# Kernel optimization log

Hardware: AMD Instinct MI355X
Metric: run time of the kernel (lower is better)

Reference implementation:

```python
import jax, jax.numpy as jnp
import numpy as np

GAMMA = 1.0
BIG = 1e10  # finite stand-in for +inf so exp/log stay NaN-free under autodiff


def _pairwise_sq_dist(X, Y):
    # X: (na, T, d), Y: (nb, T, d) -> D: (na, nb, T, T) squared euclidean
    sqx = jnp.sum(X * X, axis=-1)                      # (na, T)
    sqy = jnp.sum(Y * Y, axis=-1)                      # (nb, T)
    cross = jnp.einsum('atd,bsd->abts', X, Y)          # (na, nb, T, T)
    return sqx[:, None, :, None] + sqy[None, :, None, :] - 2.0 * cross


def _soft_dtw(D, gamma):
    # D: (B, T, T) -> (B,) soft-DTW values, anti-diagonal wavefront via lax.scan.
    B, T, _ = D.shape
    inv_g = 1.0 / gamma
    idx = jnp.arange(T)

    def step(carry, p):
        prev2, prev1 = carry                           # diagonals p-2, p-1: (B, T)
        j = p - idx
        valid = (j >= 0) & (j < T)
        d = D[:, idx, jnp.clip(j, 0, T - 1)]           # (B, T) costs on diag p
        # shifted neighbors: prev2[i-1] (diag), prev1[i-1] (up), prev1[i] (left)
        corner = jnp.where(p == 0, 0.0, BIG)           # R[0,0] = 0 boundary
        prev2_s = jnp.concatenate([jnp.broadcast_to(corner, (B, 1)), prev2[:, :-1]], axis=1)
        prev1_s = jnp.concatenate([jnp.full((B, 1), BIG, D.dtype), prev1[:, :-1]], axis=1)
        r0 = -prev2_s * inv_g
        r1 = -prev1_s * inv_g
        r2 = -prev1 * inv_g
        rmax = jnp.maximum(jnp.maximum(r0, r1), r2)
        rsum = jnp.exp(r0 - rmax) + jnp.exp(r1 - rmax) + jnp.exp(r2 - rmax)
        softmin = -gamma * (jnp.log(rsum) + rmax)
        new = jnp.where(valid[None, :], d + softmin, BIG)
        return (prev1, new), None

    init = (jnp.full((B, T), BIG, D.dtype), jnp.full((B, T), BIG, D.dtype))
    (_, last), _ = jax.lax.scan(step, init, jnp.arange(2 * T - 1))
    return last[:, T - 1]                              # R[T, T]


def setup_inputs() -> dict:
    key = jax.random.key(0)
    kx, ky = jax.random.split(key)
    X = jax.random.normal(kx, (128, 128, 8), dtype=jnp.float32)
    Y = jax.random.normal(ky, (16, 128, 8), dtype=jnp.float32)
    return {"X": X, "Y": Y}


def reference(X, Y):
    na, T, _ = X.shape
    nb = Y.shape[0]
    D = _pairwise_sq_dist(X, Y).reshape(na * nb, T, T)
    dist = _soft_dtw(D, GAMMA)
    return dist.reshape(na, nb)
```

## Files before the change

### kernel.cpp

```cpp
#include <hip/hip_runtime.h>

#define T 128
#define L2E 1.4426950408889634f
#define LN2F 0.6931471805599453f

typedef _Float16 h2 __attribute__((ext_vector_type(2)));

__device__ __forceinline__ float shr1(float x) {
    return __int_as_float(__builtin_amdgcn_update_dpp(
        0, __float_as_int(x), 0x138, 0xF, 0xF, true));
}

template <int CTRL>
__device__ __forceinline__ float dppmax(float x) {
    float t = __int_as_float(__builtin_amdgcn_update_dpp(
        __float_as_int(x), __float_as_int(x), CTRL, 0xF, 0xF, false));
    return fmaxf(x, t);
}

struct Row { float2 u, v; float s; };

__device__ __forceinline__ Row loadRow(const float* p) {
    Row r;
    r.u = *(const float2*)p;
    r.v = *(const float2*)(p + 2);
    r.s = p[4];
    return r;
}

__device__ __forceinline__ float dot2(h2 x, float ybits, float acc) {
    return __builtin_amdgcn_fdot2(x, __builtin_bit_cast(h2, ybits), acc, false);
}

__launch_bounds__(256)
__global__ void sdtw_kernel(const float* __restrict__ X,
                            const float* __restrict__ Y,
                            float* __restrict__ out) {
    __shared__ __align__(16) float lds[4 * 2304];
    const int lane = threadIdx.x & 63;
    const int w    = threadIdx.x >> 6;
    const int pair = blockIdx.x * 4 + w;
    const int a = pair >> 4;
    const int b = pair & 15;

    float* yw = lds + w * 2304;

    {
        const float* ybase = Y + (size_t)b * T * 8;
        for (int r = lane; r < 383; r += 64) {
            float4 pk; pk.x = 0.f; pk.y = 0.f; pk.z = 0.f; pk.w = 0.f;
            float sq = -3.0e37f;
            int j = r - 126;
            if (j >= 0 && j < T) {
                const float4* src = (const float4*)(ybase + j * 8);
                float4 y0 = src[0], y1 = src[1];
                float s = y0.x*y0.x + y0.y*y0.y + y0.z*y0.z + y0.w*y0.w
                        + y1.x*y1.x + y1.y*y1.y + y1.z*y1.z + y1.w*y1.w;
                const float c = 2.0f * L2E;
                h2 a0 = { (_Float16)(c*y0.x), (_Float16)(c*y0.y) };
                h2 a1 = { (_Float16)(c*y0.z), (_Float16)(c*y0.w) };
                h2 a2 = { (_Float16)(c*y1.x), (_Float16)(c*y1.y) };
                h2 a3 = { (_Float16)(c*y1.z), (_Float16)(c*y1.w) };
                pk.x = __builtin_bit_cast(float, a0);
                pk.y = __builtin_bit_cast(float, a1);
                pk.z = __builtin_bit_cast(float, a2);
                pk.w = __builtin_bit_cast(float, a3);
                sq = -L2E * s;
            }
            float* dst = yw + r * 6;
            float2 h; h.x = pk.x; h.y = pk.y;
            float2 g; g.x = pk.z; g.y = pk.w;
            *(float2*)dst = h;
            *(float2*)(dst + 2) = g;
            dst[4] = sq;
        }
    }

    h2 xe0, xe1, xe2, xe3, xo0, xo1, xo2, xo3;
    float lsxe, lsxo;
    {
        const float* xb = X + ((size_t)a * T + 2 * lane) * 8;
        const float4* s0 = (const float4*)xb;
        float4 v0 = s0[0], v1 = s0[1], u0 = s0[2], u1 = s0[3];
        xe0 = h2{ (_Float16)v0.x, (_Float16)v0.y };
        xe1 = h2{ (_Float16)v0.z, (_Float16)v0.w };
        xe2 = h2{ (_Float16)v1.x, (_Float16)v1.y };
        xe3 = h2{ (_Float16)v1.z, (_Float16)v1.w };
        lsxe = -L2E * (v0.x*v0.x+v0.y*v0.y+v0.z*v0.z+v0.w*v0.w
                      +v1.x*v1.x+v1.y*v1.y+v1.z*v1.z+v1.w*v1.w);
        xo0 = h2{ (_Float16)u0.x, (_Float16)u0.y };
        xo1 = h2{ (_Float16)u0.z, (_Float16)u0.w };
        xo2 = h2{ (_Float16)u1.x, (_Float16)u1.y };
        xo3 = h2{ (_Float16)u1.z, (_Float16)u1.w };
        lsxo = -L2E * (u0.x*u0.x+u0.y*u0.y+u0.z*u0.z+u0.w*u0.w
                      +u1.x*u1.x+u1.y*u1.y+u1.z*u1.z+u1.w*u1.w);
    }

    __syncthreads();

    Row ra = loadRow(yw + (126 - 2 * lane) * 6);
    Row rb = loadRow(yw + (127 - 2 * lane) * 6);
    Row rc = loadRow(yw + (128 - 2 * lane) * 6);
    Row rd;
    const float* fptr = yw + (129 - 2 * lane) * 6;

    float fe0 = 0.f, fo0 = 0.f, fo1 = 0.f;
    int off = 90;
    float fe1;
    {
        float acc = lsxe + ra.s;
        acc = dot2(xe0, ra.u.x, acc);
        acc = dot2(xe1, ra.u.y, acc);
        acc = dot2(xe2, ra.v.x, acc);
        acc = dot2(xe3, ra.v.y, acc);
        fe1 = __builtin_amdgcn_exp2f(acc) * 0x1p90f;
    }

#define BODY(PE1, PE2, PO1, PO2, RO, RE, RF) {          \
    RF = loadRow(fptr); fptr += 6;                      \
    float sB = shr1(PO1);                               \
    float sA = shr1(PO2);                               \
    float ae = lsxe + RE.s;                             \
    ae = dot2(xe0, RE.u.x, ae);                         \
    ae = dot2(xe1, RE.u.y, ae);                         \
    ae = dot2(xe2, RE.v.x, ae);                         \
    ae = dot2(xe3, RE.v.y, ae);                         \
    float ao = lsxo + RO.s;                             \
    ao = dot2(xo0, RO.u.x, ao);                         \
    ao = dot2(xo1, RO.u.y, ao);                         \
    ao = dot2(xo2, RO.v.x, ao);                         \
    ao = dot2(xo3, RO.v.y, ao);                         \
    float Ee = __builtin_amdgcn_exp2f(ae);              \
    float Eo = __builtin_amdgcn_exp2f(ao);              \
    float Se = Ee * ((sA + sB) + PE1);                  \
    float So = Eo * ((PE2 + PE1) + PO1);                \
    PE2 = Se; PO2 = So;                                 \
}

#define RENORM() {                                                            \
    float mx = fmaxf(fmaxf(fe0, fe1), fmaxf(fo0, fo1));                       \
    mx = dppmax<0x111>(mx);                                    \
    mx = dppmax<0x112>(mx);                                    \
    mx = dppmax<0x114>(mx);                                    \
    mx = dppmax<0x118>(mx);                                    \
    int r0_ = __builtin_amdgcn_readlane(__float_as_int(mx), 15);              \
    int r1_ = __builtin_amdgcn_readlane(__float_as_int(mx), 31);              \
    int r2_ = __builtin_amdgcn_readlane(__float_as_int(mx), 47);              \
    int r3_ = __builtin_amdgcn_readlane(__float_as_int(mx), 63);              \
    int mb = max(max(r0_, r1_), max(r2_, r3_));                               \
    int e = ((mb >> 23) & 0xff) - 217;                \
    fe0 = ldexpf(fe0, -e); fe1 = ldexpf(fe1, -e);                             \
    fo0 = ldexpf(fo0, -e); fo1 = ldexpf(fo1, -e);                             \
    off -= e;                                                                 \
}

    for (int g = 0; g < 63; ++g) {
        BODY(fe1, fe0, fo1, fo0, ra, rb, rd);
        BODY(fe0, fe1, fo0, fo1, rb, rc, ra);
        BODY(fe1, fe0, fo1, fo0, rc, rd, rb);
        BODY(fe0, fe1, fo0, fo1, rd, ra, rc);
        RENORM();
    }
    BODY(fe1, fe0, fo1, fo0, ra, rb, rd);
    BODY(fe0, fe1, fo0, fo1, rb, rc, ra);

    if (lane == 63)
        out[pair] = ((float)off - __builtin_amdgcn_logf(fo1)) * LN2F;
}

extern "C" void kernel_launch(void* const* d_in, const int* in_sizes, int n_in,
                              void* d_out, int out_size, void* d_ws, size_t ws_size,
                              hipStream_t stream) {
    const float* X = (const float*)d_in[0];
    const float* Y = (const float*)d_in[1];
    float* out = (float*)d_out;
    sdtw_kernel<<<512, 256, 0, stream>>>(X, Y, out);
}
```

Before: 86.50 us.

## Software-pipeline distance/exp stage ahead of recurrence with split even/odd LDS layout

Moves the Y-row LDS table into separate even/odd float4 arrays plus scalar arrays, so each row is read with one 16-byte load and one scalar load instead of three loads. The dot-product and exp2 for the next diagonal step are computed one step ahead of the serial recurrence, taking that latency off the loop-carried dependency chain. Each dot product is also split into two independent accumulator chains to shorten latency. In exchange it uses more registers for the extra prefetched row sets and the precomputed exponentials.

```diff
diff --git a/kernel.cpp b/kernel.cpp
--- a/kernel.cpp
+++ b/kernel.cpp
@@ -18,39 +18,38 @@
     return fmaxf(x, t);
 }
 
-struct Row { float2 u, v; float s; };
-
-__device__ __forceinline__ Row loadRow(const float* p) {
-    Row r;
-    r.u = *(const float2*)p;
-    r.v = *(const float2*)(p + 2);
-    r.s = p[4];
-    return r;
-}
-
 __device__ __forceinline__ float dot2(h2 x, float ybits, float acc) {
     return __builtin_amdgcn_fdot2(x, __builtin_bit_cast(h2, ybits), acc, false);
 }
+
+struct Pair { float4 ye; float se; float4 yo; float so; };
 
 __launch_bounds__(256)
 __global__ void sdtw_kernel(const float* __restrict__ X,
                             const float* __restrict__ Y,
                             float* __restrict__ out) {
-    __shared__ __align__(16) float lds[4 * 2304];
+    __shared__ float4 EYs[4][196];
+    __shared__ float  ESs[4][196];
+    __shared__ float4 OYs[4][196];
+    __shared__ float  OSs[4][196];
     const int lane = threadIdx.x & 63;
     const int w    = threadIdx.x >> 6;
     const int pair = blockIdx.x * 4 + w;
     const int a = pair >> 4;
     const int b = pair & 15;
 
-    float* yw = lds + w * 2304;
+    const float4* eyw = EYs[w];
+    const float*  esw = ESs[w];
+    const float4* oyw = OYs[w];
+    const float*  osw = OSs[w];
 
     {
         const float* ybase = Y + (size_t)b * T * 8;
-        for (int r = lane; r < 383; r += 64) {
+        for (int idx = lane; idx < 392; idx += 64) {
+            int P = idx & 1, h = idx >> 1;
+            int j = 2 * h + P - 126;
             float4 pk; pk.x = 0.f; pk.y = 0.f; pk.z = 0.f; pk.w = 0.f;
             float sq = -3.0e37f;
-            int j = r - 126;
             if (j >= 0 && j < T) {
                 const float4* src = (const float4*)(ybase + j * 8);
                 float4 y0 = src[0], y1 = src[1];
@@ -67,12 +66,8 @@
                 pk.w = __builtin_bit_cast(float, a3);
                 sq = -L2E * s;
             }
-            float* dst = yw + r * 6;
-            float2 h; h.x = pk.x; h.y = pk.y;
-            float2 g; g.x = pk.z; g.y = pk.w;
-            *(float2*)dst = h;
-            *(float2*)(dst + 2) = g;
-            dst[4] = sq;
+            if (P) { OYs[w][h] = pk; OSs[w][h] = sq; }
+            else   { EYs[w][h] = pk; ESs[w][h] = sq; }
         }
     }
 
@@ -80,8 +75,8 @@
     float lsxe, lsxo;
     {
         const float* xb = X + ((size_t)a * T + 2 * lane) * 8;
-        const float4* s0 = (const float4*)xb;
-        float4 v0 = s0[0], v1 = s0[1], u0 = s0[2], u1 = s0[3];
+        const float4* s0p = (const float4*)xb;
+        float4 v0 = s0p[0], v1 = s0p[1], u0 = s0p[2], u1 = s0p[3];
         xe0 = h2{ (_Float16)v0.x, (_Float16)v0.y };
         xe1 = h2{ (_Float16)v0.z, (_Float16)v0.w };
         xe2 = h2{ (_Float16)v1.x, (_Float16)v1.y };
@@ -98,43 +93,32 @@
 
     __syncthreads();
 
-    Row ra = loadRow(yw + (126 - 2 * lane) * 6);
-    Row rb = loadRow(yw + (127 - 2 * lane) * 6);
-    Row rc = loadRow(yw + (128 - 2 * lane) * 6);
-    Row rd;
-    const float* fptr = yw + (129 - 2 * lane) * 6;
+    const int hb0 = 63 - lane;
 
-    float fe0 = 0.f, fo0 = 0.f, fo1 = 0.f;
-    int off = 90;
-    float fe1;
-    {
-        float acc = lsxe + ra.s;
-        acc = dot2(xe0, ra.u.x, acc);
-        acc = dot2(xe1, ra.u.y, acc);
-        acc = dot2(xe2, ra.v.x, acc);
-        acc = dot2(xe3, ra.v.y, acc);
-        fe1 = __builtin_amdgcn_exp2f(acc) * 0x1p90f;
-    }
+#define LD_OE(SET, HE, HO) { SET.ye = oyw[HE]; SET.se = osw[HE]; \
+                             SET.yo = eyw[HO]; SET.so = esw[HO]; }
+#define LD_EO(SET, HE, HO) { SET.ye = eyw[HE]; SET.se = esw[HE]; \
+                             SET.yo = oyw[HO]; SET.so = osw[HO]; }
 
-#define BODY(PE1, PE2, PO1, PO2, RO, RE, RF) {          \
-    RF = loadRow(fptr); fptr += 6;                      \
-    float sB = shr1(PO1);                               \
-    float sA = shr1(PO2);                               \
-    float ae = lsxe + RE.s;                             \
-    ae = dot2(xe0, RE.u.x, ae);                         \
-    ae = dot2(xe1, RE.u.y, ae);                         \
-    ae = dot2(xe2, RE.v.x, ae);                         \
-    ae = dot2(xe3, RE.v.y, ae);                         \
-    float ao = lsxo + RO.s;                             \
-    ao = dot2(xo0, RO.u.x, ao);                         \
-    ao = dot2(xo1, RO.u.y, ao);                         \
-    ao = dot2(xo2, RO.v.x, ao);                         \
-    ao = dot2(xo3, RO.v.y, ao);                         \
-    float Ee = __builtin_amdgcn_exp2f(ae);              \
-    float Eo = __builtin_amdgcn_exp2f(ao);              \
-    float Se = Ee * ((sA + sB) + PE1);                  \
-    float So = Eo * ((PE2 + PE1) + PO1);                \
-    PE2 = Se; PO2 = So;                                 \
+#define DSTAGE(EE, EO, SET) {                                \
+    float t0 = dot2(xe0, SET.ye.x, lsxe);                    \
+    float t1 = dot2(xe1, SET.ye.y, SET.se);                  \
+    t0 = dot2(xe2, SET.ye.z, t0);                            \
+    t1 = dot2(xe3, SET.ye.w, t1);                            \
+    EE = __builtin_amdgcn_exp2f(t0 + t1);                    \
+    float u0 = dot2(xo0, SET.yo.x, lsxo);                    \
+    float u1 = dot2(xo1, SET.yo.y, SET.so);                  \
+    u0 = dot2(xo2, SET.yo.z, u0);                            \
+    u1 = dot2(xo3, SET.yo.w, u1);                            \
+    EO = __builtin_amdgcn_exp2f(u0 + u1);                    \
+}
+
+#define RSTAGE(PE1, PE2, PO1, PO2, EE, EO) {                 \
+    float sB = shr1(PO1);                                    \
+    float sA = shr1(PO2);                                    \
+    float Se = EE * ((sA + sB) + PE1);                       \
+    float So = EO * ((PE2 + PE1) + PO1);                     \
+    PE2 = Se; PO2 = So;                                      \
 }
 
 #define RENORM() {                                                            \
@@ -154,15 +138,47 @@
     off -= e;                                                                 \
 }
 
+    Pair S1, S2, S3, S4;
+    LD_OE(S1, hb0,     hb0);
+    LD_EO(S2, hb0 + 1, hb0);
+    LD_OE(S3, hb0 + 1, hb0 + 1);
+    LD_EO(S4, hb0 + 2, hb0 + 1);
+
+    float fe0 = 0.f, fo0 = 0.f, fo1 = 0.f, fe1;
+    int off = 90;
+    {
+        float4 yv = eyw[hb0];
+        float  sv = esw[hb0];
+        float t0 = dot2(xe0, yv.x, lsxe);
+        float t1 = dot2(xe1, yv.y, sv);
+        t0 = dot2(xe2, yv.z, t0);
+        t1 = dot2(xe3, yv.w, t1);
+        fe1 = __builtin_amdgcn_exp2f(t0 + t1) * 0x1p90f;
+    }
+    float EeA, EoA, EeB, EoB;
+    DSTAGE(EeA, EoA, S1);
+
+    int hb = hb0;
     for (int g = 0; g < 63; ++g) {
-        BODY(fe1, fe0, fo1, fo0, ra, rb, rd);
-        BODY(fe0, fe1, fo0, fo1, rb, rc, ra);
-        BODY(fe1, fe0, fo1, fo0, rc, rd, rb);
-        BODY(fe0, fe1, fo0, fo1, rd, ra, rc);
+        RSTAGE(fe1, fe0, fo1, fo0, EeA, EoA);
+        DSTAGE(EeB, EoB, S2);
+        LD_OE(S1, hb + 2, hb + 2);
+        RSTAGE(fe0, fe1, fo0, fo1, EeB, EoB);
+        DSTAGE(EeA, EoA, S3);
+        LD_EO(S2, hb + 3, hb + 2);
+        RSTAGE(fe1, fe0, fo1, fo0, EeA, EoA);
+        DSTAGE(EeB, EoB, S4);
+        LD_OE(S3, hb + 3, hb + 3);
+        RSTAGE(fe0, fe1, fo0, fo1, EeB, EoB);
+        DSTAGE(EeA, EoA, S1);
+        LD_EO(S4, hb + 4, hb + 3);
         RENORM();
+        hb += 2;
     }
-    BODY(fe1, fe0, fo1, fo0, ra, rb, rd);
-    BODY(fe0, fe1, fo0, fo1, rb, rc, ra);
+
+    RSTAGE(fe1, fe0, fo1, fo0, EeA, EoA);
+    DSTAGE(EeB, EoB, S2);
+    RSTAGE(fe0, fe1, fo0, fo1, EeB, EoB);
 
     if (lane == 63)
         out[pair] = ((float)off - __builtin_amdgcn_logf(fo1)) * LN2F;
```

Measured after the change: 88.91 us. +2.8%, slower.

## Stream Y rows through lanes via DPP shift instead of per-lane LDS loads

Applied to the files above, without the earlier changes.

Replaces the per-lane, per-step LDS row loads at lane-dependent offsets with a shift register. The Y rows ripple across lanes through DPP row-shift merges, and only lane 0 takes a fresh row, which all lanes read as a broadcast from the same LDS address. LDS rows are padded to 8 floats and batched as 8 wave-uniform loads per group, separated from the compute by a sched_barrier. The dot products are split into two independent accumulators to shorten the dependency chain. In exchange, each step adds five DPP moves and more register pressure from the eight preloaded rows.

```diff
diff --git a/kernel.cpp b/kernel.cpp
--- a/kernel.cpp
+++ b/kernel.cpp
@@ -3,12 +3,18 @@
 #define T 128
 #define L2E 1.4426950408889634f
 #define LN2F 0.6931471805599453f
+#define SENT -3.0e37f
 
 typedef _Float16 h2 __attribute__((ext_vector_type(2)));
 
 __device__ __forceinline__ float shr1(float x) {
     return __int_as_float(__builtin_amdgcn_update_dpp(
         0, __float_as_int(x), 0x138, 0xF, 0xF, true));
+}
+
+__device__ __forceinline__ float mrg(float fresh, float chain) {
+    return __int_as_float(__builtin_amdgcn_update_dpp(
+        __float_as_int(fresh), __float_as_int(chain), 0x138, 0xF, 0xF, false));
 }
 
 template <int CTRL>
@@ -18,41 +24,33 @@
     return fmaxf(x, t);
 }
 
-struct Row { float2 u, v; float s; };
-
-__device__ __forceinline__ Row loadRow(const float* p) {
-    Row r;
-    r.u = *(const float2*)p;
-    r.v = *(const float2*)(p + 2);
-    r.s = p[4];
-    return r;
-}
-
 __device__ __forceinline__ float dot2(h2 x, float ybits, float acc) {
     return __builtin_amdgcn_fdot2(x, __builtin_bit_cast(h2, ybits), acc, false);
 }
+
+struct Row { float4 y; float s; };
 
 __launch_bounds__(256)
 __global__ void sdtw_kernel(const float* __restrict__ X,
                             const float* __restrict__ Y,
                             float* __restrict__ out) {
-    __shared__ __align__(16) float lds[4 * 2304];
+    __shared__ __align__(16) float lds[4][2048];
     const int lane = threadIdx.x & 63;
     const int w    = threadIdx.x >> 6;
     const int pair = blockIdx.x * 4 + w;
     const int a = pair >> 4;
     const int b = pair & 15;
 
-    float* yw = lds + w * 2304;
+    float* yw = lds[w];
 
     {
         const float* ybase = Y + (size_t)b * T * 8;
-        for (int r = lane; r < 383; r += 64) {
+        for (int k = 0; k < 4; ++k) {
+            int r = lane + 64 * k;
             float4 pk; pk.x = 0.f; pk.y = 0.f; pk.z = 0.f; pk.w = 0.f;
-            float sq = -3.0e37f;
-            int j = r - 126;
-            if (j >= 0 && j < T) {
-                const float4* src = (const float4*)(ybase + j * 8);
+            float sq = SENT;
+            if (r < T) {
+                const float4* src = (const float4*)(ybase + r * 8);
                 float4 y0 = src[0], y1 = src[1];
                 float s = y0.x*y0.x + y0.y*y0.y + y0.z*y0.z + y0.w*y0.w
                         + y1.x*y1.x + y1.y*y1.y + y1.z*y1.z + y1.w*y1.w;
@@ -67,12 +65,10 @@
                 pk.w = __builtin_bit_cast(float, a3);
                 sq = -L2E * s;
             }
-            float* dst = yw + r * 6;
-            float2 h; h.x = pk.x; h.y = pk.y;
-            float2 g; g.x = pk.z; g.y = pk.w;
-            *(float2*)dst = h;
-            *(float2*)(dst + 2) = g;
-            dst[4] = sq;
+            float* dst = yw + r * 8;
+            *(float4*)dst = pk;
+            float4 t; t.x = sq; t.y = 0.f; t.z = 0.f; t.w = 0.f;
+            *(float4*)(dst + 4) = t;
         }
     }
 
@@ -80,8 +76,8 @@
     float lsxe, lsxo;
     {
         const float* xb = X + ((size_t)a * T + 2 * lane) * 8;
-        const float4* s0 = (const float4*)xb;
-        float4 v0 = s0[0], v1 = s0[1], u0 = s0[2], u1 = s0[3];
+        const float4* s0p = (const float4*)xb;
+        float4 v0 = s0p[0], v1 = s0p[1], u0 = s0p[2], u1 = s0p[3];
         xe0 = h2{ (_Float16)v0.x, (_Float16)v0.y };
         xe1 = h2{ (_Float16)v0.z, (_Float16)v0.w };
         xe2 = h2{ (_Float16)v1.x, (_Float16)v1.y };
@@ -98,43 +94,58 @@
 
     __syncthreads();
 
-    Row ra = loadRow(yw + (126 - 2 * lane) * 6);
-    Row rb = loadRow(yw + (127 - 2 * lane) * 6);
-    Row rc = loadRow(yw + (128 - 2 * lane) * 6);
-    Row rd;
-    const float* fptr = yw + (129 - 2 * lane) * 6;
-
-    float fe0 = 0.f, fo0 = 0.f, fo1 = 0.f;
+    Row A, B;
+    {
+        float4 r0y = *(const float4*)(yw);
+        float  r0s = yw[4];
+        bool l0 = (lane == 0);
+        A.y.x = l0 ? r0y.x : 0.f;
+        A.y.y = l0 ? r0y.y : 0.f;
+        A.y.z = l0 ? r0y.z : 0.f;
+        A.y.w = l0 ? r0y.w : 0.f;
+        A.s   = l0 ? r0s   : SENT;
+        B.y.x = 0.f; B.y.y = 0.f; B.y.z = 0.f; B.y.w = 0.f;
+        B.s   = SENT;
+    }
+
+    float fe0 = 0.f, fo0 = 0.f, fo1 = 0.f, fe1;
     int off = 90;
-    float fe1;
-    {
-        float acc = lsxe + ra.s;
-        acc = dot2(xe0, ra.u.x, acc);
-        acc = dot2(xe1, ra.u.y, acc);
-        acc = dot2(xe2, ra.v.x, acc);
-        acc = dot2(xe3, ra.v.y, acc);
-        fe1 = __builtin_amdgcn_exp2f(acc) * 0x1p90f;
-    }
-
-#define BODY(PE1, PE2, PO1, PO2, RO, RE, RF) {          \
-    RF = loadRow(fptr); fptr += 6;                      \
+    {
+        float t0 = dot2(xe0, A.y.x, lsxe);
+        float t1 = dot2(xe1, A.y.y, A.s);
+        t0 = dot2(xe2, A.y.z, t0);
+        t1 = dot2(xe3, A.y.w, t1);
+        fe1 = __builtin_amdgcn_exp2f(t0 + t1) * 0x1p90f;
+    }
+    {
+        float4 fy = *(const float4*)(yw + 8);
+        float  fs = yw[12];
+        B.y.x = mrg(fy.x, B.y.x); B.y.y = mrg(fy.y, B.y.y);
+        B.y.z = mrg(fy.z, B.y.z); B.y.w = mrg(fy.w, B.y.w);
+        B.s   = mrg(fs,   B.s);
+    }
+
+#define BODY(PE1, PE2, PO1, PO2, RE, RO, F) {           \
+    float t0 = dot2(xe0, RE.y.x, lsxe);                 \
+    float t1 = dot2(xe1, RE.y.y, RE.s);                 \
+    t0 = dot2(xe2, RE.y.z, t0);                         \
+    t1 = dot2(xe3, RE.y.w, t1);                         \
+    float Ee = __builtin_amdgcn_exp2f(t0 + t1);         \
+    float u0 = dot2(xo0, RO.y.x, lsxo);                 \
+    float u1 = dot2(xo1, RO.y.y, RO.s);                 \
+    u0 = dot2(xo2, RO.y.z, u0);                         \
+    u1 = dot2(xo3, RO.y.w, u1);                         \
+    float Eo = __builtin_amdgcn_exp2f(u0 + u1);         \
     float sB = shr1(PO1);                               \
     float sA = shr1(PO2);                               \
-    float ae = lsxe + RE.s;                             \
-    ae = dot2(xe0, RE.u.x, ae);                         \
-    ae = dot2(xe1, RE.u.y, ae);                         \
-    ae = dot2(xe2, RE.v.x, ae);                         \
-    ae = dot2(xe3, RE.v.y, ae);                         \
-    float ao = lsxo + RO.s;                             \
-    ao = dot2(xo0, RO.u.x, ao);                         \
-    ao = dot2(xo1, RO.u.y, ao);                         \
-    ao = dot2(xo2, RO.v.x, ao);                         \
-    ao = dot2(xo3, RO.v.y, ao);                         \
-    float Ee = __builtin_amdgcn_exp2f(ae);              \
-    float Eo = __builtin_amdgcn_exp2f(ao);              \
     float Se = Ee * ((sA + sB) + PE1);                  \
     float So = Eo * ((PE2 + PE1) + PO1);                \
     PE2 = Se; PO2 = So;                                 \
+    RO.y.x = mrg(F.y.x, RO.y.x);                        \
+    RO.y.y = mrg(F.y.y, RO.y.y);                        \
+    RO.y.z = mrg(F.y.z, RO.y.z);                        \
+    RO.y.w = mrg(F.y.w, RO.y.w);                        \
+    RO.s   = mrg(F.s,   RO.s);                          \
 }
 
 #define RENORM() {                                                            \
@@ -154,15 +165,40 @@
     off -= e;                                                                 \
 }
 
-    for (int g = 0; g < 63; ++g) {
-        BODY(fe1, fe0, fo1, fo0, ra, rb, rd);
-        BODY(fe0, fe1, fo0, fo1, rb, rc, ra);
-        BODY(fe1, fe0, fo1, fo0, rc, rd, rb);
-        BODY(fe0, fe1, fo0, fo1, rd, ra, rc);
+#define LOADF(F, OFS) { F.y = *(const float4*)(gb + (OFS)); F.s = gb[(OFS) + 4]; }
+
+    int rb = 16;
+    for (int g = 0; g < 31; ++g) {
+        const float* gb = yw + rb;
+        Row F0, F1, F2, F3, F4, F5, F6, F7;
+        LOADF(F0, 0);  LOADF(F1, 8);  LOADF(F2, 16); LOADF(F3, 24);
+        LOADF(F4, 32); LOADF(F5, 40); LOADF(F6, 48); LOADF(F7, 56);
+        __builtin_amdgcn_sched_barrier(0);
+        BODY(fe1, fe0, fo1, fo0, B, A, F0);
+        BODY(fe0, fe1, fo0, fo1, A, B, F1);
+        BODY(fe1, fe0, fo1, fo0, B, A, F2);
+        BODY(fe0, fe1, fo0, fo1, A, B, F3);
+        BODY(fe1, fe0, fo1, fo0, B, A, F4);
+        BODY(fe0, fe1, fo0, fo1, A, B, F5);
+        BODY(fe1, fe0, fo1, fo0, B, A, F6);
+        BODY(fe0, fe1, fo0, fo1, A, B, F7);
         RENORM();
-    }
-    BODY(fe1, fe0, fo1, fo0, ra, rb, rd);
-    BODY(fe0, fe1, fo0, fo1, rb, rc, ra);
+        rb += 64;
+    }
+
+    {
+        const float* gb = yw + rb;
+        Row F0, F1, F2, F3, F4, F5;
+        LOADF(F0, 0);  LOADF(F1, 8);  LOADF(F2, 16);
+        LOADF(F3, 24); LOADF(F4, 32); LOADF(F5, 40);
+        __builtin_amdgcn_sched_barrier(0);
+        BODY(fe1, fe0, fo1, fo0, B, A, F0);
+        BODY(fe0, fe1, fo0, fo1, A, B, F1);
+        BODY(fe1, fe0, fo1, fo0, B, A, F2);
+        BODY(fe0, fe1, fo0, fo1, A, B, F3);
+        BODY(fe1, fe0, fo1, fo0, B, A, F4);
+        BODY(fe0, fe1, fo0, fo1, A, B, F5);
+    }
 
     if (lane == 63)
         out[pair] = ((float)off - __builtin_amdgcn_logf(fo1)) * LN2F;
```

After: 87.80 us. No clear change (+1.5%).

## Repack Y into paired odd/even LDS entries and reuse shifted neighbor across steps

Applied to the files above, without the earlier changes.

Lays out the per-wave Y table as interleaved entries that hold both the odd and even rows a lane needs in one 48-byte record. Each step then does a single contiguous LDS fetch instead of a Row load per step. The second DPP shift is replaced by carrying the previous shifted value in a register (sPrev), which is renormalized along with the other state. Renormalization now runs every 8 steps instead of every 4. The costs are more LDS per block, a more complex index scheme with clamped reads, and a bigger gap between renorms, which could risk overflow.

```diff
diff --git a/kernel.cpp b/kernel.cpp
--- a/kernel.cpp
+++ b/kernel.cpp
@@ -3,6 +3,7 @@
 #define T 128
 #define L2E 1.4426950408889634f
 #define LN2F 0.6931471805599453f
+#define SENT -3.0e37f
 
 typedef _Float16 h2 __attribute__((ext_vector_type(2)));
 
@@ -18,61 +19,70 @@
     return fmaxf(x, t);
 }
 
-struct Row { float2 u, v; float s; };
-
-__device__ __forceinline__ Row loadRow(const float* p) {
-    Row r;
-    r.u = *(const float2*)p;
-    r.v = *(const float2*)(p + 2);
-    r.s = p[4];
-    return r;
-}
-
 __device__ __forceinline__ float dot2(h2 x, float ybits, float acc) {
     return __builtin_amdgcn_fdot2(x, __builtin_bit_cast(h2, ybits), acc, false);
 }
+
+struct Ent { float4 yo, ye; float so, se; };
 
 __launch_bounds__(256)
 __global__ void sdtw_kernel(const float* __restrict__ X,
                             const float* __restrict__ Y,
                             float* __restrict__ out) {
-    __shared__ __align__(16) float lds[4 * 2304];
+    __shared__ __align__(16) float lds[4 * 3180];
     const int lane = threadIdx.x & 63;
     const int w    = threadIdx.x >> 6;
     const int pair = blockIdx.x * 4 + w;
     const int a = pair >> 4;
     const int b = pair & 15;
 
-    float* yw = lds + w * 2304;
+    float* EA = lds + w * 3180;
+    float* EB = EA + 133 * 12;
 
     {
         const float* ybase = Y + (size_t)b * T * 8;
-        for (int r = lane; r < 383; r += 64) {
-            float4 pk; pk.x = 0.f; pk.y = 0.f; pk.z = 0.f; pk.w = 0.f;
-            float sq = -3.0e37f;
-            int j = r - 126;
-            if (j >= 0 && j < T) {
-                const float4* src = (const float4*)(ybase + j * 8);
+        for (int idx = lane; idx < 265; idx += 64) {
+            int isB = (idx >= 133);
+            int k = isB ? idx - 133 : idx;
+            int rO = 2 * k + isB;
+            int rE = rO + 1;
+            float4 pkO, pkE;
+            pkO.x=0.f; pkO.y=0.f; pkO.z=0.f; pkO.w=0.f;
+            pkE.x=0.f; pkE.y=0.f; pkE.z=0.f; pkE.w=0.f;
+            float sqO = SENT, sqE = SENT;
+            const float c = 2.0f * L2E;
+            int jO = rO - 126, jE = rE - 126;
+            if (jO >= 0 && jO < T) {
+                const float4* src = (const float4*)(ybase + jO * 8);
                 float4 y0 = src[0], y1 = src[1];
-                float s = y0.x*y0.x + y0.y*y0.y + y0.z*y0.z + y0.w*y0.w
-                        + y1.x*y1.x + y1.y*y1.y + y1.z*y1.z + y1.w*y1.w;
-                const float c = 2.0f * L2E;
-                h2 a0 = { (_Float16)(c*y0.x), (_Float16)(c*y0.y) };
-                h2 a1 = { (_Float16)(c*y0.z), (_Float16)(c*y0.w) };
-                h2 a2 = { (_Float16)(c*y1.x), (_Float16)(c*y1.y) };
-                h2 a3 = { (_Float16)(c*y1.z), (_Float16)(c*y1.w) };
-                pk.x = __builtin_bit_cast(float, a0);
-                pk.y = __builtin_bit_cast(float, a1);
-                pk.z = __builtin_bit_cast(float, a2);
-                pk.w = __builtin_bit_cast(float, a3);
-                sq = -L2E * s;
+                float s = y0.x*y0.x+y0.y*y0.y+y0.z*y0.z+y0.w*y0.w
+                        + y1.x*y1.x+y1.y*y1.y+y1.z*y1.z+y1.w*y1.w;
+                h2 a0={(_Float16)(c*y0.x),(_Float16)(c*y0.y)};
+                h2 a1={(_Float16)(c*y0.z),(_Float16)(c*y0.w)};
+                h2 a2={(_Float16)(c*y1.x),(_Float16)(c*y1.y)};
+                h2 a3={(_Float16)(c*y1.z),(_Float16)(c*y1.w)};
+                pkO.x=__builtin_bit_cast(float,a0); pkO.y=__builtin_bit_cast(float,a1);
+                pkO.z=__builtin_bit_cast(float,a2); pkO.w=__builtin_bit_cast(float,a3);
+                sqO = -L2E * s;
             }
-            float* dst = yw + r * 6;
-            float2 h; h.x = pk.x; h.y = pk.y;
-            float2 g; g.x = pk.z; g.y = pk.w;
-            *(float2*)dst = h;
-            *(float2*)(dst + 2) = g;
-            dst[4] = sq;
+            if (jE >= 0 && jE < T) {
+                const float4* src = (const float4*)(ybase + jE * 8);
+                float4 y0 = src[0], y1 = src[1];
+                float s = y0.x*y0.x+y0.y*y0.y+y0.z*y0.z+y0.w*y0.w
+                        + y1.x*y1.x+y1.y*y1.y+y1.z*y1.z+y1.w*y1.w;
+                h2 a0={(_Float16)(c*y0.x),(_Float16)(c*y0.y)};
+                h2 a1={(_Float16)(c*y0.z),(_Float16)(c*y0.w)};
+                h2 a2={(_Float16)(c*y1.x),(_Float16)(c*y1.y)};
+                h2 a3={(_Float16)(c*y1.z),(_Float16)(c*y1.w)};
+                pkE.x=__builtin_bit_cast(float,a0); pkE.y=__builtin_bit_cast(float,a1);
+                pkE.z=__builtin_bit_cast(float,a2); pkE.w=__builtin_bit_cast(float,a3);
+                sqE = -L2E * s;
+            }
+            float* dst = (isB ? EB : EA) + k * 12;
+            *(float4*)dst       = pkO;
+            *(float4*)(dst + 4) = pkE;
+            float2 sq2; sq2.x = sqO; sq2.y = sqE;
+            *(float2*)(dst + 8) = sq2;
         }
     }
 
@@ -80,8 +90,8 @@
     float lsxe, lsxo;
     {
         const float* xb = X + ((size_t)a * T + 2 * lane) * 8;
-        const float4* s0 = (const float4*)xb;
-        float4 v0 = s0[0], v1 = s0[1], u0 = s0[2], u1 = s0[3];
+        const float4* s0p = (const float4*)xb;
+        float4 v0 = s0p[0], v1 = s0p[1], u0 = s0p[2], u1 = s0p[3];
         xe0 = h2{ (_Float16)v0.x, (_Float16)v0.y };
         xe1 = h2{ (_Float16)v0.z, (_Float16)v0.w };
         xe2 = h2{ (_Float16)v1.x, (_Float16)v1.y };
@@ -98,51 +108,47 @@
 
     __syncthreads();
 
-    Row ra = loadRow(yw + (126 - 2 * lane) * 6);
-    Row rb = loadRow(yw + (127 - 2 * lane) * 6);
-    Row rc = loadRow(yw + (128 - 2 * lane) * 6);
-    Row rd;
-    const float* fptr = yw + (129 - 2 * lane) * 6;
+#define FA(S, K) { const float* q_ = EA + min((K), 132) * 12;                 \
+    S.yo = *(const float4*)q_; S.ye = *(const float4*)(q_ + 4);               \
+    float2 sq_ = *(const float2*)(q_ + 8); S.so = sq_.x; S.se = sq_.y; }
+#define FB(S, K) { const float* q_ = EB + min((K), 131) * 12;                 \
+    S.yo = *(const float4*)q_; S.ye = *(const float4*)(q_ + 4);               \
+    float2 sq_ = *(const float2*)(q_ + 8); S.so = sq_.x; S.se = sq_.y; }
 
-    float fe0 = 0.f, fo0 = 0.f, fo1 = 0.f;
+    Ent s1, s2, s3, s4;
+    const int k0 = 63 - lane;
+    FA(s1, k0); FB(s2, k0); FA(s3, k0 + 1); FB(s4, k0 + 1);
+    int kA = k0 + 2, kB = k0 + 2;
+
+    float fe0 = 0.f, fo0 = 0.f, fo1 = 0.f, fe1;
+    float sPrev = 0.f;
     int off = 90;
-    float fe1;
     {
-        float acc = lsxe + ra.s;
-        acc = dot2(xe0, ra.u.x, acc);
-        acc = dot2(xe1, ra.u.y, acc);
-        acc = dot2(xe2, ra.v.x, acc);
-        acc = dot2(xe3, ra.v.y, acc);
+        float acc = dot2(xe3, s1.yo.w, dot2(xe2, s1.yo.z,
+                    dot2(xe1, s1.yo.y, dot2(xe0, s1.yo.x, lsxe + s1.so))));
         fe1 = __builtin_amdgcn_exp2f(acc) * 0x1p90f;
     }
 
-#define BODY(PE1, PE2, PO1, PO2, RO, RE, RF) {          \
-    RF = loadRow(fptr); fptr += 6;                      \
-    float sB = shr1(PO1);                               \
-    float sA = shr1(PO2);                               \
-    float ae = lsxe + RE.s;                             \
-    ae = dot2(xe0, RE.u.x, ae);                         \
-    ae = dot2(xe1, RE.u.y, ae);                         \
-    ae = dot2(xe2, RE.v.x, ae);                         \
-    ae = dot2(xe3, RE.v.y, ae);                         \
-    float ao = lsxo + RO.s;                             \
-    ao = dot2(xo0, RO.u.x, ao);                         \
-    ao = dot2(xo1, RO.u.y, ao);                         \
-    ao = dot2(xo2, RO.v.x, ao);                         \
-    ao = dot2(xo3, RO.v.y, ao);                         \
-    float Ee = __builtin_amdgcn_exp2f(ae);              \
-    float Eo = __builtin_amdgcn_exp2f(ao);              \
-    float Se = Ee * ((sA + sB) + PE1);                  \
-    float So = Eo * ((PE2 + PE1) + PO1);                \
-    PE2 = Se; PO2 = So;                                 \
+#define BODY(PE1, PE2, PO1, PO2, S) {                                         \
+    float ae = dot2(xe3, S.ye.w, dot2(xe2, S.ye.z,                            \
+               dot2(xe1, S.ye.y, dot2(xe0, S.ye.x, lsxe + S.se))));           \
+    float ao = dot2(xo3, S.yo.w, dot2(xo2, S.yo.z,                            \
+               dot2(xo1, S.yo.y, dot2(xo0, S.yo.x, lsxo + S.so))));           \
+    float Ee = __builtin_amdgcn_exp2f(ae);                                    \
+    float Eo = __builtin_amdgcn_exp2f(ao);                                    \
+    float sB = shr1(PO1);                                                     \
+    float Se = Ee * ((sPrev + sB) + PE1);                                     \
+    float So = Eo * ((PE2 + PE1) + PO1);                                      \
+    sPrev = sB;                                                               \
+    PE2 = Se; PO2 = So;                                                       \
 }
 
 #define RENORM() {                                                            \
     float mx = fmaxf(fmaxf(fe0, fe1), fmaxf(fo0, fo1));                       \
-    mx = dppmax<0x111>(mx);                                    \
-    mx = dppmax<0x112>(mx);                                    \
-    mx = dppmax<0x114>(mx);                                    \
-    mx = dppmax<0x118>(mx);                                    \
+    mx = dppmax<0x111>(mx);                                                   \
+    mx = dppmax<0x112>(mx);                                                   \
+    mx = dppmax<0x114>(mx);                                                   \
+    mx = dppmax<0x118>(mx);                                                   \
     int r0_ = __builtin_amdgcn_readlane(__float_as_int(mx), 15);              \
     int r1_ = __builtin_amdgcn_readlane(__float_as_int(mx), 31);              \
     int r2_ = __builtin_amdgcn_readlane(__float_as_int(mx), 47);              \
@@ -151,18 +157,29 @@
     int e = ((mb >> 23) & 0xff) - 217;                \
     fe0 = ldexpf(fe0, -e); fe1 = ldexpf(fe1, -e);                             \
     fo0 = ldexpf(fo0, -e); fo1 = ldexpf(fo1, -e);                             \
+    sPrev = ldexpf(sPrev, -e);                                                \
     off -= e;                                                                 \
 }
 
-    for (int g = 0; g < 63; ++g) {
-        BODY(fe1, fe0, fo1, fo0, ra, rb, rd);
-        BODY(fe0, fe1, fo0, fo1, rb, rc, ra);
-        BODY(fe1, fe0, fo1, fo0, rc, rd, rb);
-        BODY(fe0, fe1, fo0, fo1, rd, ra, rc);
+    for (int g = 0; g < 31; ++g) {
+        BODY(fe1, fe0, fo1, fo0, s1); FA(s1, kA);
+        BODY(fe0, fe1, fo0, fo1, s2); FB(s2, kB);
+        BODY(fe1, fe0, fo1, fo0, s3); FA(s3, kA + 1);
+        BODY(fe0, fe1, fo0, fo1, s4); FB(s4, kB + 1);
+        BODY(fe1, fe0, fo1, fo0, s1); FA(s1, kA + 2);
+        BODY(fe0, fe1, fo0, fo1, s2); FB(s2, kB + 2);
+        BODY(fe1, fe0, fo1, fo0, s3); FA(s3, kA + 3);
+        BODY(fe0, fe1, fo0, fo1, s4); FB(s4, kB + 3);
         RENORM();
+        kA += 4; kB += 4;
     }
-    BODY(fe1, fe0, fo1, fo0, ra, rb, rd);
-    BODY(fe0, fe1, fo0, fo1, rb, rc, ra);
+
+    BODY(fe1, fe0, fo1, fo0, s1); FA(s1, kA);
+    BODY(fe0, fe1, fo0, fo1, s2); FB(s2, kB);
+    BODY(fe1, fe0, fo1, fo0, s3);
+    BODY(fe0, fe1, fo0, fo1, s4);
+    BODY(fe1, fe0, fo1, fo0, s1);
+    BODY(fe0, fe1, fo0, fo1, s2);
 
     if (lane == 63)
         out[pair] = ((float)off - __builtin_amdgcn_logf(fo1)) * LN2F;
```

Measured after the change: 96.29 us. 1.11x slower.
